# Kernel tuning notes

Measured on AMD Instinct MI355X. Metric: run time of the kernel, lower is better.

The kernel has to match this reference:

```python
import jax, jax.numpy as jnp
import numpy as np

B, L = 256, 50            # batch, n_pos (session length)
ITEM_DIM, POS_DIM = 128, 64
DIM = ITEM_DIM + POS_DIM  # 192
N_ITEMS = 50000
W = 20.0                  # temperature / init scale
LN_EPS = 1e-5


def renorm(t, max_norm=1.5):
    # torch Embedding max_norm semantics: clip row L2 norm to max_norm
    n = jnp.linalg.norm(t, axis=-1, keepdims=True)
    return t * jnp.minimum(1.0, max_norm / jnp.maximum(n, 1e-7))


def setup_inputs() -> dict:
    key = jax.random.key(0)
    ks = jax.random.split(key, 24)
    inv_w = 1.0 / W
    lb = 1.0 / np.sqrt(DIM)
    lb3 = 1.0 / np.sqrt(3 * DIM)
    u = lambda k, shape, b: jax.random.uniform(k, shape, jnp.float32, -b, b)
    emb = jax.random.normal(ks[0], (N_ITEMS, ITEM_DIM), jnp.float32).at[0].set(0.0)
    pos_emb = jax.random.normal(ks[1], (L + 1, POS_DIM), jnp.float32).at[0].set(0.0)
    return {
        'x': jax.random.randint(ks[20], (B, L), 0, N_ITEMS),
        'pos': jnp.sort(jax.random.randint(ks[21], (B, L), 1, L + 1), axis=-1),
        'emb': emb,
        'pos_emb': pos_emb,
        'vw0': jax.random.normal(ks[2], (1, DIM), jnp.float32) * inv_w,
        'vw1': jax.random.normal(ks[3], (DIM, DIM), jnp.float32) * inv_w,
        'vw2': jax.random.normal(ks[4], (DIM, DIM), jnp.float32) * inv_w,
        'vbias': jnp.zeros((DIM,), jnp.float32),
        'w1_W': u(ks[5], (DIM, DIM), lb), 'w1_b': u(ks[6], (DIM,), lb),
        'w2_W': u(ks[7], (DIM, DIM), lb), 'w2_b': u(ks[8], (DIM,), lb),
        'wA': jax.random.normal(ks[9], (1, L), jnp.float32) * inv_w,
        'wg1_W': u(ks[10], (DIM, DIM), lb), 'wg1_b': u(ks[11], (DIM,), lb),
        'wg2_W': u(ks[12], (DIM, DIM), lb), 'wg2_b': u(ks[13], (DIM,), lb),
        'gq': jax.random.normal(ks[14], (DIM, 1), jnp.float32) * inv_w,
        'wf_W': u(ks[15], (ITEM_DIM, 3 * DIM), lb3), 'wf_b': u(ks[16], (ITEM_DIM,), lb3),
        'ln_g': jnp.ones((DIM,), jnp.float32), 'ln_b': jnp.zeros((DIM,), jnp.float32),
    }


def reference(x, pos, emb, pos_emb, vw0, vw1, vw2, vbias, w1_W, w1_b, w2_W, w2_b,
              wA, wg1_W, wg1_b, wg2_W, wg2_b, gq, wf_W, wf_b, ln_g, ln_b):
    emb_r = renorm(emb)
    x_e = emb_r[x]                                   # [B,L,item_dim]
    p_e = renorm(pos_emb)[pos]                       # [B,L,pos_dim]
    x_ = jnp.concatenate([x_e, p_e], axis=-1)        # [B,L,D]
    mask = (x != 0)                                  # [B,L]

    # --- vanila (additive) attention, all n_pos targets in one fused pass ---
    K = x_ @ vw1                                     # [B,L,D]  (shared across targets)
    Q = x_ @ vw2                                     # [B,L,D]
    h = jax.nn.relu(K[:, None, :, :] + Q[:, :, None, :] + vbias)   # [B,Li,Lj,D]
    alpha = jnp.einsum('bijd,d->bij', h, vw0[0])     # scores over keys j
    alpha = jnp.where(mask[:, None, :], alpha, -jnp.inf)
    a = jax.nn.softmax(alpha, axis=-1)
    S = jnp.einsum('bij,bjd->bid', a, x_)            # [B,L,D]

    # --- MLP + LayerNorm + position mixing ---
    h2 = jax.nn.relu(S @ w1_W.T + w1_b)
    S2 = h2 @ w2_W.T + w2_b + S
    mu = jnp.mean(S2, axis=-1, keepdims=True)
    var = jnp.mean((S2 - mu) ** 2, axis=-1, keepdims=True)
    S3 = ln_g * (S2 - mu) * jax.lax.rsqrt(var + LN_EPS) + ln_b
    st = jnp.einsum('p,bpd->bd', wA[0], S3)[:, None, :]   # [B,1,D]

    # --- global attention ---
    sl = x_[:, -1:, :]                               # [B,1,D]
    g = jax.nn.sigmoid(x_ @ wg1_W.T + wg1_b + (sl @ wg2_W.T + wg2_b))
    ag = g @ gq                                      # [B,L,1]
    sg = jnp.einsum('blo,bld->bod', ag, x_)          # [B,1,D]

    # --- decoder: cosine-similarity logits against item embeddings ---
    c = jax.nn.selu(jnp.concatenate([st, sl, sg], axis=-1) @ wf_W.T + wf_b)[:, 0, :]
    c = c / jnp.linalg.norm(c, axis=-1, keepdims=True)
    le = emb_r[1:]
    le = le / jnp.linalg.norm(le, axis=-1, keepdims=True)
    z = W * (c @ le.T)                               # [B, n_items-1]
    return z
```

## Files before the change

kernel.cpp:

```cpp
#include <hip/hip_runtime.h>
#include <hip/hip_bf16.h>
#include <math.h>
#include <stdint.h>

#define BB 256
#define LL 50
#define IDIM 128
#define PDIM 64
#define DIM 192
#define NITEMS 50000
#define NOUT 49999
#define WSC 20.0f
#define EPS 1e-5f
#define WMAT (DIM * DIM)

typedef __attribute__((ext_vector_type(8))) short  short8;
typedef __attribute__((ext_vector_type(4))) float  f32x4;

__device__ __forceinline__ unsigned short f2bf(float f) {
    unsigned int u = __float_as_uint(f);
    u = (u + 0x7FFFu + ((u >> 16) & 1u)) >> 16;
    return (unsigned short)u;
}
__device__ __forceinline__ float bf2f(unsigned short u) {
    unsigned int v = ((unsigned int)u) << 16;
    return __uint_as_float(v);
}

__global__ __launch_bounds__(256) void k_norms(const float* __restrict__ emb,
                                               float* __restrict__ scale,
                                               float* __restrict__ invn,
                                               unsigned short* __restrict__ emb16) {
    int row  = blockIdx.x * 4 + (threadIdx.x >> 6);
    int lane = threadIdx.x & 63;
    const float* p = emb + (size_t)row * IDIM;
    float a = p[lane], b = p[lane + 64];
    emb16[(size_t)row * IDIM + lane]      = f2bf(a);
    emb16[(size_t)row * IDIM + lane + 64] = f2bf(b);
    float s = a * a + b * b;
#pragma unroll
    for (int off = 32; off; off >>= 1) s += __shfl_xor(s, off);
    if (lane == 0) {
        float n = sqrtf(s);
        scale[row] = fminf(1.0f, 1.5f / fmaxf(n, 1e-7f));
        invn[row]  = (n > 0.f) ? 1.f / n : 0.f;
    }
}

__global__ __launch_bounds__(64) void k_pnorms(const float* __restrict__ pe,
                                               float* __restrict__ pscale) {
    int row = threadIdx.x;
    if (row > LL) return;
    float s = 0.f;
    const float* p = pe + row * PDIM;
    for (int d = 0; d < PDIM; ++d) { float v = p[d]; s += v * v; }
    float n = sqrtf(s);
    pscale[row] = fminf(1.0f, 1.5f / fmaxf(n, 1e-7f));
}

__global__ __launch_bounds__(256) void k_cvtw(const float* __restrict__ vw1, const float* __restrict__ vw2,
                                              const float* __restrict__ w1W, const float* __restrict__ w2W,
                                              const float* __restrict__ wg1W,
                                              unsigned short* __restrict__ Wout) {
    int b = blockIdx.x;
    int wi = b / 144;
    int pos = (b % 144) * 256 + threadIdx.x;
    int n = pos / DIM, k = pos - n * DIM;
    float v;
    if      (wi == 0) v = vw1[(size_t)k * DIM + n];
    else if (wi == 1) v = vw2[(size_t)k * DIM + n];
    else if (wi == 2) v = w1W[pos];
    else if (wi == 3) v = w2W[pos];
    else              v = wg1W[pos];
    Wout[(size_t)wi * WMAT + pos] = f2bf(v);
}

__global__ __launch_bounds__(512) void k_mega(
    const int* __restrict__ x, const int* __restrict__ pos,
    const float* __restrict__ emb, const float* __restrict__ pe,
    const float* __restrict__ scale, const float* __restrict__ pscale,
    const unsigned short* __restrict__ W16,
    const float* __restrict__ vw0, const float* __restrict__ vbias,
    const float* __restrict__ w1b, const float* __restrict__ w2b,
    const float* __restrict__ wg1b, const float* __restrict__ wg2W,
    const float* __restrict__ wg2b, const float* __restrict__ gq,
    const float* __restrict__ wA, const float* __restrict__ lng,
    const float* __restrict__ lnb, const float* __restrict__ wfW,
    const float* __restrict__ wfb, unsigned short* __restrict__ Cb16g) {

    __shared__ unsigned short Bs16[64 * DIM];
    __shared__ unsigned short X16T[DIM * 72];
    __shared__ unsigned short Ab16[64 * 72];
    __shared__ float R1[LL * 196];
    __shared__ float R2[LL * 196];
    __shared__ float xlast[DIM];
    __shared__ float GLs[DIM];
    __shared__ float cvec[3 * DIM];
    __shared__ float red2[4][128];
    __shared__ float ags[64];
    __shared__ int   msk[64];
    __shared__ float was[64];
    __shared__ float red[8];
    __shared__ int   xi[LL], pii[LL];
    __shared__ float xsc[LL], psc[LL];

    const int b = blockIdx.x, t = threadIdx.x;
    const int wv = t >> 6, l = t & 63;
    const int lr = l & 15, lk = l >> 4;

    if (t < LL) {
        int v = x[b * LL + t];  xi[t] = v;  xsc[t] = scale[v];
        int pv = pos[b * LL + t]; pii[t] = pv; psc[t] = pscale[pv];
    }
    if (t >= 64 && t < 128) ags[t - 64] = 0.f;
    if (t >= 128 && t < 128 + LL) was[t - 128] = wA[t - 128];
    __syncthreads();
    if (t < 64) msk[t] = (t < LL) ? xi[t] : 0;
    for (int r = wv; r < LL; r += 8) {
        float sx = xsc[r], sp = psc[r];
        float v0 = emb[(size_t)xi[r] * IDIM + l] * sx;
        float v1 = emb[(size_t)xi[r] * IDIM + l + 64] * sx;
        float v2 = pe[pii[r] * PDIM + l] * sp;
        int base = r * 384, sw = (r & 7) << 4;
        *(unsigned short*)((char*)Bs16 + ((base + l * 2) ^ sw))         = f2bf(v0);
        *(unsigned short*)((char*)Bs16 + ((base + (l + 64) * 2) ^ sw))  = f2bf(v1);
        *(unsigned short*)((char*)Bs16 + ((base + (l + 128) * 2) ^ sw)) = f2bf(v2);
        X16T[l * 72 + r]         = f2bf(v0);
        X16T[(l + 64) * 72 + r]  = f2bf(v1);
        X16T[(l + 128) * 72 + r] = f2bf(v2);
        if (r == 49) { xlast[l] = v0; xlast[l + 64] = v1; xlast[l + 128] = v2; }
    }
    for (int e = t; e < 14 * DIM; e += 512) Bs16[LL * DIM + e] = 0;
    for (int e = t; e < DIM * 14; e += 512) { int d = e / 14, j = 50 + (e - d * 14); X16T[d * 72 + j] = 0; }
    for (int e = t; e < 14 * 72; e += 512) Ab16[50 * 72 + e] = 0;
    __syncthreads();

    if (t < DIM) {
        float g = wg2b[t];
        const float* wr = wg2W + (size_t)t * DIM;
        float s0 = 0, s1 = 0, s2 = 0, s3 = 0;
        for (int k = 0; k < DIM; k += 4) {
            float4 w4 = *(const float4*)(wr + k);
            s0 += xlast[k] * w4.x; s1 += xlast[k + 1] * w4.y;
            s2 += xlast[k + 2] * w4.z; s3 += xlast[k + 3] * w4.w;
        }
        GLs[t] = g + ((s0 + s1) + (s2 + s3));
    }
    __syncthreads();

    {
        short8 afr[4][6];
#pragma unroll
        for (int mt = 0; mt < 4; ++mt) {
            int row = mt * 16 + lr;
#pragma unroll
            for (int ks = 0; ks < 6; ++ks) {
                int byte = (row * 384 + (lk * 8 + ks * 32) * 2) ^ ((row & 7) << 4);
                afr[mt][ks] = *(const short8*)((const char*)Bs16 + byte);
            }
        }
        for (int task = wv; task < 36; task += 8) {
            int out = task / 12, nt = task % 12;
            int ncol = nt * 16 + lr;
            const unsigned short* bp = W16 + (size_t)(out == 0 ? 0 : (out == 1 ? 1 : 4)) * WMAT
                                       + (size_t)ncol * DIM + lk * 8;
            f32x4 a0 = {}, a1 = {}, a2 = {}, a3 = {};
#pragma unroll
            for (int ks = 0; ks < 6; ++ks) {
                short8 bf = *(const short8*)(bp + ks * 32);
                a0 = __builtin_amdgcn_mfma_f32_16x16x32_bf16(afr[0][ks], bf, a0, 0, 0, 0);
                a1 = __builtin_amdgcn_mfma_f32_16x16x32_bf16(afr[1][ks], bf, a1, 0, 0, 0);
                a2 = __builtin_amdgcn_mfma_f32_16x16x32_bf16(afr[2][ks], bf, a2, 0, 0, 0);
                a3 = __builtin_amdgcn_mfma_f32_16x16x32_bf16(afr[3][ks], bf, a3, 0, 0, 0);
            }
            if (out == 0) {
                float bia = vbias[ncol];
#pragma unroll
                for (int mt = 0; mt < 4; ++mt) {
                    f32x4 ac = (mt == 0) ? a0 : (mt == 1) ? a1 : (mt == 2) ? a2 : a3;
#pragma unroll
                    for (int r = 0; r < 4; ++r) {
                        int gr = mt * 16 + lk * 4 + r;
                        if (gr < LL) R1[gr * 196 + ncol] = ac[r] + bia;
                    }
                }
            } else if (out == 1) {
#pragma unroll
                for (int mt = 0; mt < 4; ++mt) {
                    f32x4 ac = (mt == 0) ? a0 : (mt == 1) ? a1 : (mt == 2) ? a2 : a3;
#pragma unroll
                    for (int r = 0; r < 4; ++r) {
                        int gr = mt * 16 + lk * 4 + r;
                        if (gr < LL) R2[gr * 196 + ncol] = ac[r];
                    }
                }
            } else {
                float bia = wg1b[ncol] + GLs[ncol];
                float gqv = gq[ncol];
#pragma unroll
                for (int mt = 0; mt < 4; ++mt) {
                    f32x4 ac = (mt == 0) ? a0 : (mt == 1) ? a1 : (mt == 2) ? a2 : a3;
                    int gr0 = mt * 16 + lk * 4;
                    float v0 = ac[0] + bia, v1 = ac[1] + bia, v2 = ac[2] + bia, v3 = ac[3] + bia;
                    float c0 = (gr0 + 0 < LL) ? gqv / (1.f + expf(-v0)) : 0.f;
                    float c1 = (gr0 + 1 < LL) ? gqv / (1.f + expf(-v1)) : 0.f;
                    float c2 = (gr0 + 2 < LL) ? gqv / (1.f + expf(-v2)) : 0.f;
                    float c3 = (gr0 + 3 < LL) ? gqv / (1.f + expf(-v3)) : 0.f;
#pragma unroll
                    for (int off = 1; off < 16; off <<= 1) {
                        c0 += __shfl_xor(c0, off); c1 += __shfl_xor(c1, off);
                        c2 += __shfl_xor(c2, off); c3 += __shfl_xor(c3, off);
                    }
                    if (lr == 0) {
                        if (gr0 + 0 < LL) atomicAdd(&ags[gr0 + 0], c0);
                        if (gr0 + 1 < LL) atomicAdd(&ags[gr0 + 1], c1);
                        if (gr0 + 2 < LL) atomicAdd(&ags[gr0 + 2], c2);
                        if (gr0 + 3 < LL) atomicAdd(&ags[gr0 + 3], c3);
                    }
                }
            }
        }
    }
    __syncthreads();

    {
        const int d0 = wv * 24;
        float kr[24], wr[24];
        {
            const float* wp = vw0 + d0;
#pragma unroll
            for (int q = 0; q < 6; ++q) {
                float4 v = *(const float4*)(wp + q * 4);
                wr[q * 4] = v.x; wr[q * 4 + 1] = v.y; wr[q * 4 + 2] = v.z; wr[q * 4 + 3] = v.w;
            }
            if (l < LL) {
                const float* kp = R1 + l * 196 + d0;
#pragma unroll
                for (int q = 0; q < 6; ++q) {
                    float4 v = *(const float4*)(kp + q * 4);
                    kr[q * 4] = v.x; kr[q * 4 + 1] = v.y; kr[q * 4 + 2] = v.z; kr[q * 4 + 3] = v.w;
                }
            } else {
#pragma unroll
                for (int q = 0; q < 24; ++q) kr[q] = 0.f;
            }
        }
        __syncthreads();
        float* parts = R1;
        const float NEG = -__builtin_inff();
        bool valid = (l < LL) && (msk[l] != 0);
        for (int i0 = 0; i0 < LL; i0 += 12) {
            int cnt = (i0 + 12 <= LL) ? 12 : (LL - i0);
            for (int i = 0; i < cnt; ++i) {
                const float* qrow = R2 + (i0 + i) * 196 + d0;
                float b0 = 0, b1 = 0, b2 = 0, b3 = 0;
#pragma unroll
                for (int q = 0; q < 6; ++q) {
                    float4 qv = *(const float4*)(qrow + q * 4);
                    b0 += fmaxf(kr[q * 4 + 0] + qv.x, 0.f) * wr[q * 4 + 0];
                    b1 += fmaxf(kr[q * 4 + 1] + qv.y, 0.f) * wr[q * 4 + 1];
                    b2 += fmaxf(kr[q * 4 + 2] + qv.z, 0.f) * wr[q * 4 + 2];
                    b3 += fmaxf(kr[q * 4 + 3] + qv.w, 0.f) * wr[q * 4 + 3];
                }
                parts[(wv * 12 + i) * 64 + l] = (b0 + b1) + (b2 + b3);
            }
            __syncthreads();
            for (int i = wv; i < cnt; i += 8) {
                float aj = 0.f;
#pragma unroll
                for (int w2 = 0; w2 < 8; ++w2) aj += parts[(w2 * 12 + i) * 64 + l];
                if (!valid) aj = NEG;
                float m = aj;
#pragma unroll
                for (int off = 32; off; off >>= 1) m = fmaxf(m, __shfl_xor(m, off));
                float e = valid ? expf(aj - m) : 0.f;
                float s = e;
#pragma unroll
                for (int off = 32; off; off >>= 1) s += __shfl_xor(s, off);
                Ab16[(i0 + i) * 72 + l] = f2bf(e / s);
            }
            __syncthreads();
        }
    }

    for (int task = wv; task < 48; task += 8) {
        int mt = task / 12, nt = task - (task / 12) * 12;
        int i0 = mt * 16, d0c = nt * 16;
        short8 aA0 = *(const short8*)(Ab16 + (i0 + lr) * 72 + lk * 8);
        short8 aA1 = *(const short8*)(Ab16 + (i0 + lr) * 72 + 32 + lk * 8);
        short8 bB0 = *(const short8*)(X16T + (d0c + lr) * 72 + lk * 8);
        short8 bB1 = *(const short8*)(X16T + (d0c + lr) * 72 + 32 + lk * 8);
        f32x4 ac = {};
        ac = __builtin_amdgcn_mfma_f32_16x16x32_bf16(aA0, bB0, ac, 0, 0, 0);
        ac = __builtin_amdgcn_mfma_f32_16x16x32_bf16(aA1, bB1, ac, 0, 0, 0);
        int d = d0c + lr;
#pragma unroll
        for (int r = 0; r < 4; ++r) {
            int i = i0 + lk * 4 + r;
            if (i < LL) {
                R2[i * 196 + d] = ac[r];
                int byte = (i * 384 + d * 2) ^ ((i & 7) << 4);
                *(unsigned short*)((char*)Bs16 + byte) = f2bf(ac[r]);
            }
        }
    }
    __syncthreads();

    {
        short8 sfr[4][6];
#pragma unroll
        for (int mt = 0; mt < 4; ++mt) {
            int row = mt * 16 + lr;
#pragma unroll
            for (int ks = 0; ks < 6; ++ks) {
                int byte = (row * 384 + (lk * 8 + ks * 32) * 2) ^ ((row & 7) << 4);
                sfr[mt][ks] = *(const short8*)((const char*)Bs16 + byte);
            }
        }
        f32x4 h0[4] = {}, h1[4] = {};
        {
            int ncol = wv * 16 + lr;
            const unsigned short* bp = W16 + (size_t)2 * WMAT + (size_t)ncol * DIM + lk * 8;
#pragma unroll
            for (int ks = 0; ks < 6; ++ks) {
                short8 bf = *(const short8*)(bp + ks * 32);
                h0[0] = __builtin_amdgcn_mfma_f32_16x16x32_bf16(sfr[0][ks], bf, h0[0], 0, 0, 0);
                h0[1] = __builtin_amdgcn_mfma_f32_16x16x32_bf16(sfr[1][ks], bf, h0[1], 0, 0, 0);
                h0[2] = __builtin_amdgcn_mfma_f32_16x16x32_bf16(sfr[2][ks], bf, h0[2], 0, 0, 0);
                h0[3] = __builtin_amdgcn_mfma_f32_16x16x32_bf16(sfr[3][ks], bf, h0[3], 0, 0, 0);
            }
        }
        if (wv < 4) {
            int ncol = (wv + 8) * 16 + lr;
            const unsigned short* bp = W16 + (size_t)2 * WMAT + (size_t)ncol * DIM + lk * 8;
#pragma unroll
            for (int ks = 0; ks < 6; ++ks) {
                short8 bf = *(const short8*)(bp + ks * 32);
                h1[0] = __builtin_amdgcn_mfma_f32_16x16x32_bf16(sfr[0][ks], bf, h1[0], 0, 0, 0);
                h1[1] = __builtin_amdgcn_mfma_f32_16x16x32_bf16(sfr[1][ks], bf, h1[1], 0, 0, 0);
                h1[2] = __builtin_amdgcn_mfma_f32_16x16x32_bf16(sfr[2][ks], bf, h1[2], 0, 0, 0);
                h1[3] = __builtin_amdgcn_mfma_f32_16x16x32_bf16(sfr[3][ks], bf, h1[3], 0, 0, 0);
            }
        }
        __syncthreads();
        {
            int gc = wv * 16 + lr;
            float bia = w1b[gc];
#pragma unroll
            for (int mt = 0; mt < 4; ++mt)
#pragma unroll
                for (int r = 0; r < 4; ++r) {
                    int gr = mt * 16 + lk * 4 + r;
                    if (gr < LL) {
                        float v = fmaxf(h0[mt][r] + bia, 0.f);
                        int byte = (gr * 384 + gc * 2) ^ ((gr & 7) << 4);
                        *(unsigned short*)((char*)Bs16 + byte) = f2bf(v);
                    }
                }
        }
        if (wv < 4) {
            int gc = (wv + 8) * 16 + lr;
            float bia = w1b[gc];
#pragma unroll
            for (int mt = 0; mt < 4; ++mt)
#pragma unroll
                for (int r = 0; r < 4; ++r) {
                    int gr = mt * 16 + lk * 4 + r;
                    if (gr < LL) {
                        float v = fmaxf(h1[mt][r] + bia, 0.f);
                        int byte = (gr * 384 + gc * 2) ^ ((gr & 7) << 4);
                        *(unsigned short*)((char*)Bs16 + byte) = f2bf(v);
                    }
                }
        }
    }
    __syncthreads();

    {
        short8 hfr[4][6];
#pragma unroll
        for (int mt = 0; mt < 4; ++mt) {
            int row = mt * 16 + lr;
#pragma unroll
            for (int ks = 0; ks < 6; ++ks) {
                int byte = (row * 384 + (lk * 8 + ks * 32) * 2) ^ ((row & 7) << 4);
                hfr[mt][ks] = *(const short8*)((const char*)Bs16 + byte);
            }
        }
        for (int nt = wv; nt < 12; nt += 8) {
            int ncol = nt * 16 + lr;
            const unsigned short* bp = W16 + (size_t)3 * WMAT + (size_t)ncol * DIM + lk * 8;
            f32x4 s0 = {}, s1 = {}, s2 = {}, s3 = {};
#pragma unroll
            for (int ks = 0; ks < 6; ++ks) {
                short8 bf = *(const short8*)(bp + ks * 32);
                s0 = __builtin_amdgcn_mfma_f32_16x16x32_bf16(hfr[0][ks], bf, s0, 0, 0, 0);
                s1 = __builtin_amdgcn_mfma_f32_16x16x32_bf16(hfr[1][ks], bf, s1, 0, 0, 0);
                s2 = __builtin_amdgcn_mfma_f32_16x16x32_bf16(hfr[2][ks], bf, s2, 0, 0, 0);
                s3 = __builtin_amdgcn_mfma_f32_16x16x32_bf16(hfr[3][ks], bf, s3, 0, 0, 0);
            }
            float bia = w2b[ncol];
#pragma unroll
            for (int mt = 0; mt < 4; ++mt) {
                f32x4 ac = (mt == 0) ? s0 : (mt == 1) ? s1 : (mt == 2) ? s2 : s3;
#pragma unroll
                for (int r = 0; r < 4; ++r) {
                    int gr = mt * 16 + lk * 4 + r;
                    if (gr < LL) R2[gr * 196 + ncol] = ac[r] + bia + R2[gr * 196 + ncol];
                }
            }
        }
    }
    __syncthreads();

    for (int r = wv; r < LL; r += 8) {
        float* p = R2 + r * 196;
        float v0 = p[l], v1 = p[l + 64], v2 = p[l + 128];
        float s = v0 + v1 + v2;
#pragma unroll
        for (int off = 32; off; off >>= 1) s += __shfl_xor(s, off);
        float mu = s * (1.f / DIM);
        float d0 = v0 - mu, d1 = v1 - mu, d2 = v2 - mu;
        float q = d0 * d0 + d1 * d1 + d2 * d2;
#pragma unroll
        for (int off = 32; off; off >>= 1) q += __shfl_xor(q, off);
        float inv = rsqrtf(q * (1.f / DIM) + EPS);
        p[l]       = lng[l] * d0 * inv + lnb[l];
        p[l + 64]  = lng[l + 64] * d1 * inv + lnb[l + 64];
        p[l + 128] = lng[l + 128] * d2 * inv + lnb[l + 128];
    }
    __syncthreads();

    if (t < DIM) {
        float st = 0.f;
        for (int p = 0; p < LL; ++p) st += was[p] * R2[p * 196 + t];
        cvec[t] = st;
        cvec[DIM + t] = xlast[t];
    } else if (t >= 320) {
        int d = t - 320;
        float sg = 0.f;
        const unsigned short* xr = X16T + d * 72;
        for (int p = 0; p < LL; ++p) sg += ags[p] * bf2f(xr[p]);
        cvec[2 * DIM + d] = sg;
    }
    __syncthreads();

    {
        int out = t & 127, part = t >> 7;
        float s = (part == 0) ? wfb[out] : 0.f;
        const float* wr = wfW + (size_t)out * (3 * DIM) + part * 144;
        const float* cv = cvec + part * 144;
        for (int e = 0; e < 144; e += 4) {
            float4 w4 = *(const float4*)(wr + e);
            s += cv[e] * w4.x + cv[e + 1] * w4.y + cv[e + 2] * w4.z + cv[e + 3] * w4.w;
        }
        red2[part][out] = s;
    }
    __syncthreads();
    float cj = 0.f;
    if (t < IDIM) {
        float s = red2[0][t] + red2[1][t] + red2[2][t] + red2[3][t];
        const float sa = 1.6732632423543772f, sc = 1.0507009873554805f;
        cj = sc * (s > 0.f ? s : sa * expm1f(s));
    }
    float sq = cj * cj;
#pragma unroll
    for (int off = 32; off; off >>= 1) sq += __shfl_xor(sq, off);
    if (l == 0) red[wv] = sq;
    __syncthreads();
    if (t < IDIM) {
        float nrm = sqrtf(red[0] + red[1]);
        Cb16g[b * IDIM + t] = f2bf(cj / nrm);
    }
}

__global__ __launch_bounds__(256) void k_z4(const unsigned short* __restrict__ Cb16,
                                            const unsigned short* __restrict__ emb16,
                                            const float* __restrict__ invn,
                                            float* __restrict__ Z) {
    __shared__ float tr[4][64][68];
    int n0 = blockIdx.x * 64;
    int t = threadIdx.x, w = t >> 6, l = t & 63;
    int lr = l & 15, lk = l >> 4;

    short8 a[4][4];
#pragma unroll
    for (int mt = 0; mt < 4; ++mt) {
        int mrow = w * 64 + mt * 16 + lr;
        const unsigned short* ap = Cb16 + (size_t)mrow * IDIM + lk * 8;
#pragma unroll
        for (int ks = 0; ks < 4; ++ks) a[mt][ks] = *(const short8*)(ap + ks * 32);
    }
    f32x4 acc[4][4] = {};
#pragma unroll
    for (int nt = 0; nt < 4; ++nt) {
        int nrow = n0 + nt * 16 + lr;
        short8 bfr[4];
        if (nrow < NOUT) {
            const unsigned short* bp = emb16 + (size_t)(nrow + 1) * IDIM + lk * 8;
#pragma unroll
            for (int ks = 0; ks < 4; ++ks) bfr[ks] = *(const short8*)(bp + ks * 32);
        } else {
            short8 z = {};
#pragma unroll
            for (int ks = 0; ks < 4; ++ks) bfr[ks] = z;
        }
#pragma unroll
        for (int mt = 0; mt < 4; ++mt)
#pragma unroll
            for (int ks = 0; ks < 4; ++ks)
                acc[mt][nt] = __builtin_amdgcn_mfma_f32_16x16x32_bf16(a[mt][ks], bfr[ks], acc[mt][nt], 0, 0, 0);
    }
#pragma unroll
    for (int nt = 0; nt < 4; ++nt) {
        int gn = n0 + nt * 16 + lr;
        float sc = (gn < NOUT) ? WSC * invn[gn + 1] : 0.f;
#pragma unroll
        for (int mt = 0; mt < 4; ++mt)
#pragma unroll
            for (int r = 0; r < 4; ++r)
                tr[w][mt * 16 + lk * 4 + r][nt * 16 + lr] = acc[mt][nt][r] * sc;
    }
    __syncthreads();
    int q = l >> 4, s = l & 15;
    bool tail = (n0 + 64) > NOUT;
#pragma unroll
    for (int it = 0; it < 16; ++it) {
        int row = it * 4 + q;
        int gm  = w * 64 + row;
        float4 v = *(const float4*)&tr[w][row][s * 4];
        if (!tail) {
            *(float4*)&Z[(size_t)gm * NOUT + n0 + s * 4] = v;
        } else {
            int c0 = n0 + s * 4;
            float vv[4] = {v.x, v.y, v.z, v.w};
#pragma unroll
            for (int j = 0; j < 4; ++j)
                if (c0 + j < NOUT) Z[(size_t)gm * NOUT + c0 + j] = vv[j];
        }
    }
}

extern "C" void kernel_launch(void* const* d_in, const int* in_sizes, int n_in,
                              void* d_out, int out_size, void* d_ws, size_t ws_size,
                              hipStream_t stream) {
    const int*   x     = (const int*)d_in[0];
    const int*   pos   = (const int*)d_in[1];
    const float* emb   = (const float*)d_in[2];
    const float* pose  = (const float*)d_in[3];
    const float* vw0   = (const float*)d_in[4];
    const float* vw1   = (const float*)d_in[5];
    const float* vw2   = (const float*)d_in[6];
    const float* vbias = (const float*)d_in[7];
    const float* w1W   = (const float*)d_in[8];
    const float* w1b   = (const float*)d_in[9];
    const float* w2W   = (const float*)d_in[10];
    const float* w2b   = (const float*)d_in[11];
    const float* wA    = (const float*)d_in[12];
    const float* wg1W  = (const float*)d_in[13];
    const float* wg1b  = (const float*)d_in[14];
    const float* wg2W  = (const float*)d_in[15];
    const float* wg2b  = (const float*)d_in[16];
    const float* gq    = (const float*)d_in[17];
    const float* wfW   = (const float*)d_in[18];
    const float* wfb   = (const float*)d_in[19];
    const float* lng   = (const float*)d_in[20];
    const float* lnb   = (const float*)d_in[21];
    float* Z = (float*)d_out;

    float* w = (float*)d_ws;
    float* scale  = w; w += NITEMS;
    float* invn   = w; w += NITEMS;
    float* pscale = w; w += 64;
    w = (float*)(((uintptr_t)w + 15) & ~(uintptr_t)15);
    unsigned short* emb16 = (unsigned short*)w; w += (size_t)NITEMS * IDIM / 2;
    unsigned short* W16   = (unsigned short*)w; w += (size_t)5 * WMAT / 2;
    unsigned short* Cb16  = (unsigned short*)w; w += (size_t)BB * IDIM / 2;

    k_norms<<<NITEMS / 4, 256, 0, stream>>>(emb, scale, invn, emb16);
    k_pnorms<<<1, 64, 0, stream>>>(pose, pscale);
    k_cvtw<<<5 * 144, 256, 0, stream>>>(vw1, vw2, w1W, w2W, wg1W, W16);
    k_mega<<<BB, 512, 0, stream>>>(x, pos, emb, pose, scale, pscale, W16,
                                   vw0, vbias, w1b, w2b, wg1b, wg2W, wg2b, gq,
                                   wA, lng, lnb, wfW, wfb, Cb16);
    k_z4<<<(NOUT + 63) / 64, 256, 0, stream>>>(Cb16, emb16, invn, Z);
}
```

Before: 109.9 us.

## Double k_mega block to 1024 threads and redistribute per-stage work across 16 waves

Launches the per-session mega kernel with 1024 threads (16 waves) instead of 512 and re-partitions each stage to use them. The two 192-column MLP GEMMs now give one 16-column tile to each of 12 waves instead of a lopsided 8+4 split. The attention-score rows are split across wave halves, and the st/sg reductions and the wf projection are split across more threads with an extra partial-sum pass. This aims to cut the serial latency of the one-block-per-batch kernel, which only launches 256 blocks, at the cost of more barriers, register pressure under launch_bounds(1024,4), and idle waves in some stages.

```diff
diff --git a/kernel.cpp b/kernel.cpp
--- a/kernel.cpp
+++ b/kernel.cpp
@@ -75,7 +75,7 @@
     Wout[(size_t)wi * WMAT + pos] = f2bf(v);
 }
 
-__global__ __launch_bounds__(512) void k_mega(
+__global__ __launch_bounds__(1024, 4) void k_mega(
     const int* __restrict__ x, const int* __restrict__ pos,
     const float* __restrict__ emb, const float* __restrict__ pe,
     const float* __restrict__ scale, const float* __restrict__ pscale,
@@ -96,11 +96,12 @@
     __shared__ float xlast[DIM];
     __shared__ float GLs[DIM];
     __shared__ float cvec[3 * DIM];
-    __shared__ float red2[4][128];
+    __shared__ float stB[DIM], sgB[DIM];
+    __shared__ float red2[8][128];
     __shared__ float ags[64];
     __shared__ int   msk[64];
     __shared__ float was[64];
-    __shared__ float red[8];
+    __shared__ float red[16];
     __shared__ int   xi[LL], pii[LL];
     __shared__ float xsc[LL], psc[LL];
 
@@ -116,7 +117,7 @@
     if (t >= 128 && t < 128 + LL) was[t - 128] = wA[t - 128];
     __syncthreads();
     if (t < 64) msk[t] = (t < LL) ? xi[t] : 0;
-    for (int r = wv; r < LL; r += 8) {
+    for (int r = wv; r < LL; r += 16) {
         float sx = xsc[r], sp = psc[r];
         float v0 = emb[(size_t)xi[r] * IDIM + l] * sx;
         float v1 = emb[(size_t)xi[r] * IDIM + l + 64] * sx;
@@ -130,9 +131,9 @@
         X16T[(l + 128) * 72 + r] = f2bf(v2);
         if (r == 49) { xlast[l] = v0; xlast[l + 64] = v1; xlast[l + 128] = v2; }
     }
-    for (int e = t; e < 14 * DIM; e += 512) Bs16[LL * DIM + e] = 0;
-    for (int e = t; e < DIM * 14; e += 512) { int d = e / 14, j = 50 + (e - d * 14); X16T[d * 72 + j] = 0; }
-    for (int e = t; e < 14 * 72; e += 512) Ab16[50 * 72 + e] = 0;
+    for (int e = t; e < 14 * DIM; e += 1024) Bs16[LL * DIM + e] = 0;
+    for (int e = t; e < DIM * 14; e += 1024) { int d = e / 14, j = 50 + (e - d * 14); X16T[d * 72 + j] = 0; }
+    for (int e = t; e < 14 * 72; e += 1024) Ab16[50 * 72 + e] = 0;
     __syncthreads();
 
     if (t < DIM) {
@@ -159,7 +160,7 @@
                 afr[mt][ks] = *(const short8*)((const char*)Bs16 + byte);
             }
         }
-        for (int task = wv; task < 36; task += 8) {
+        for (int task = wv; task < 36; task += 16) {
             int out = task / 12, nt = task % 12;
             int ncol = nt * 16 + lr;
             const unsigned short* bp = W16 + (size_t)(out == 0 ? 0 : (out == 1 ? 1 : 4)) * WMAT
@@ -224,7 +225,8 @@
     __syncthreads();
 
     {
-        const int d0 = wv * 24;
+        const int d0 = (wv & 7) * 24;
+        const int ih = wv >> 3;
         float kr[24], wr[24];
         {
             const float* wp = vw0 + d0;
@@ -251,7 +253,7 @@
         bool valid = (l < LL) && (msk[l] != 0);
         for (int i0 = 0; i0 < LL; i0 += 12) {
             int cnt = (i0 + 12 <= LL) ? 12 : (LL - i0);
-            for (int i = 0; i < cnt; ++i) {
+            for (int i = ih; i < cnt; i += 2) {
                 const float* qrow = R2 + (i0 + i) * 196 + d0;
                 float b0 = 0, b1 = 0, b2 = 0, b3 = 0;
 #pragma unroll
@@ -262,10 +264,10 @@
                     b2 += fmaxf(kr[q * 4 + 2] + qv.z, 0.f) * wr[q * 4 + 2];
                     b3 += fmaxf(kr[q * 4 + 3] + qv.w, 0.f) * wr[q * 4 + 3];
                 }
-                parts[(wv * 12 + i) * 64 + l] = (b0 + b1) + (b2 + b3);
+                parts[((wv & 7) * 12 + i) * 64 + l] = (b0 + b1) + (b2 + b3);
             }
             __syncthreads();
-            for (int i = wv; i < cnt; i += 8) {
+            for (int i = wv; i < cnt; i += 16) {
                 float aj = 0.f;
 #pragma unroll
                 for (int w2 = 0; w2 < 8; ++w2) aj += parts[(w2 * 12 + i) * 64 + l];
@@ -283,7 +285,7 @@
         }
     }
 
-    for (int task = wv; task < 48; task += 8) {
+    for (int task = wv; task < 48; task += 16) {
         int mt = task / 12, nt = task - (task / 12) * 12;
         int i0 = mt * 16, d0c = nt * 16;
         short8 aA0 = *(const short8*)(Ab16 + (i0 + lr) * 72 + lk * 8);
@@ -308,17 +310,17 @@
 
     {
         short8 sfr[4][6];
-#pragma unroll
-        for (int mt = 0; mt < 4; ++mt) {
-            int row = mt * 16 + lr;
-#pragma unroll
-            for (int ks = 0; ks < 6; ++ks) {
-                int byte = (row * 384 + (lk * 8 + ks * 32) * 2) ^ ((row & 7) << 4);
-                sfr[mt][ks] = *(const short8*)((const char*)Bs16 + byte);
-            }
-        }
-        f32x4 h0[4] = {}, h1[4] = {};
-        {
+        f32x4 h0[4] = {};
+        if (wv < 12) {
+#pragma unroll
+            for (int mt = 0; mt < 4; ++mt) {
+                int row = mt * 16 + lr;
+#pragma unroll
+                for (int ks = 0; ks < 6; ++ks) {
+                    int byte = (row * 384 + (lk * 8 + ks * 32) * 2) ^ ((row & 7) << 4);
+                    sfr[mt][ks] = *(const short8*)((const char*)Bs16 + byte);
+                }
+            }
             int ncol = wv * 16 + lr;
             const unsigned short* bp = W16 + (size_t)2 * WMAT + (size_t)ncol * DIM + lk * 8;
 #pragma unroll
@@ -330,20 +332,8 @@
                 h0[3] = __builtin_amdgcn_mfma_f32_16x16x32_bf16(sfr[3][ks], bf, h0[3], 0, 0, 0);
             }
         }
-        if (wv < 4) {
-            int ncol = (wv + 8) * 16 + lr;
-            const unsigned short* bp = W16 + (size_t)2 * WMAT + (size_t)ncol * DIM + lk * 8;
-#pragma unroll
-            for (int ks = 0; ks < 6; ++ks) {
-                short8 bf = *(const short8*)(bp + ks * 32);
-                h1[0] = __builtin_amdgcn_mfma_f32_16x16x32_bf16(sfr[0][ks], bf, h1[0], 0, 0, 0);
-                h1[1] = __builtin_amdgcn_mfma_f32_16x16x32_bf16(sfr[1][ks], bf, h1[1], 0, 0, 0);
-                h1[2] = __builtin_amdgcn_mfma_f32_16x16x32_bf16(sfr[2][ks], bf, h1[2], 0, 0, 0);
-                h1[3] = __builtin_amdgcn_mfma_f32_16x16x32_bf16(sfr[3][ks], bf, h1[3], 0, 0, 0);
-            }
-        }
         __syncthreads();
-        {
+        if (wv < 12) {
             int gc = wv * 16 + lr;
             float bia = w1b[gc];
 #pragma unroll
@@ -358,25 +348,10 @@
                     }
                 }
         }
-        if (wv < 4) {
-            int gc = (wv + 8) * 16 + lr;
-            float bia = w1b[gc];
-#pragma unroll
-            for (int mt = 0; mt < 4; ++mt)
-#pragma unroll
-                for (int r = 0; r < 4; ++r) {
-                    int gr = mt * 16 + lk * 4 + r;
-                    if (gr < LL) {
-                        float v = fmaxf(h1[mt][r] + bia, 0.f);
-                        int byte = (gr * 384 + gc * 2) ^ ((gr & 7) << 4);
-                        *(unsigned short*)((char*)Bs16 + byte) = f2bf(v);
-                    }
-                }
-        }
-    }
-    __syncthreads();
-
-    {
+    }
+    __syncthreads();
+
+    if (wv < 12) {
         short8 hfr[4][6];
 #pragma unroll
         for (int mt = 0; mt < 4; ++mt) {
@@ -387,33 +362,31 @@
                 hfr[mt][ks] = *(const short8*)((const char*)Bs16 + byte);
             }
         }
-        for (int nt = wv; nt < 12; nt += 8) {
-            int ncol = nt * 16 + lr;
-            const unsigned short* bp = W16 + (size_t)3 * WMAT + (size_t)ncol * DIM + lk * 8;
-            f32x4 s0 = {}, s1 = {}, s2 = {}, s3 = {};
-#pragma unroll
-            for (int ks = 0; ks < 6; ++ks) {
-                short8 bf = *(const short8*)(bp + ks * 32);
-                s0 = __builtin_amdgcn_mfma_f32_16x16x32_bf16(hfr[0][ks], bf, s0, 0, 0, 0);
-                s1 = __builtin_amdgcn_mfma_f32_16x16x32_bf16(hfr[1][ks], bf, s1, 0, 0, 0);
-                s2 = __builtin_amdgcn_mfma_f32_16x16x32_bf16(hfr[2][ks], bf, s2, 0, 0, 0);
-                s3 = __builtin_amdgcn_mfma_f32_16x16x32_bf16(hfr[3][ks], bf, s3, 0, 0, 0);
-            }
-            float bia = w2b[ncol];
-#pragma unroll
-            for (int mt = 0; mt < 4; ++mt) {
-                f32x4 ac = (mt == 0) ? s0 : (mt == 1) ? s1 : (mt == 2) ? s2 : s3;
-#pragma unroll
-                for (int r = 0; r < 4; ++r) {
-                    int gr = mt * 16 + lk * 4 + r;
-                    if (gr < LL) R2[gr * 196 + ncol] = ac[r] + bia + R2[gr * 196 + ncol];
-                }
-            }
-        }
-    }
-    __syncthreads();
-
-    for (int r = wv; r < LL; r += 8) {
+        int ncol = wv * 16 + lr;
+        const unsigned short* bp = W16 + (size_t)3 * WMAT + (size_t)ncol * DIM + lk * 8;
+        f32x4 s0 = {}, s1 = {}, s2 = {}, s3 = {};
+#pragma unroll
+        for (int ks = 0; ks < 6; ++ks) {
+            short8 bf = *(const short8*)(bp + ks * 32);
+            s0 = __builtin_amdgcn_mfma_f32_16x16x32_bf16(hfr[0][ks], bf, s0, 0, 0, 0);
+            s1 = __builtin_amdgcn_mfma_f32_16x16x32_bf16(hfr[1][ks], bf, s1, 0, 0, 0);
+            s2 = __builtin_amdgcn_mfma_f32_16x16x32_bf16(hfr[2][ks], bf, s2, 0, 0, 0);
+            s3 = __builtin_amdgcn_mfma_f32_16x16x32_bf16(hfr[3][ks], bf, s3, 0, 0, 0);
+        }
+        float bia = w2b[ncol];
+#pragma unroll
+        for (int mt = 0; mt < 4; ++mt) {
+            f32x4 ac = (mt == 0) ? s0 : (mt == 1) ? s1 : (mt == 2) ? s2 : s3;
+#pragma unroll
+            for (int r = 0; r < 4; ++r) {
+                int gr = mt * 16 + lk * 4 + r;
+                if (gr < LL) R2[gr * 196 + ncol] = ac[r] + bia + R2[gr * 196 + ncol];
+            }
+        }
+    }
+    __syncthreads();
+
+    for (int r = wv; r < LL; r += 16) {
         float* p = R2 + r * 196;
         float v0 = p[l], v1 = p[l + 64], v2 = p[l + 128];
         float s = v0 + v1 + v2;
@@ -433,24 +406,40 @@
 
     if (t < DIM) {
         float st = 0.f;
-        for (int p = 0; p < LL; ++p) st += was[p] * R2[p * 196 + t];
+        for (int p = 0; p < 25; ++p) st += was[p] * R2[p * 196 + t];
         cvec[t] = st;
         cvec[DIM + t] = xlast[t];
-    } else if (t >= 320) {
-        int d = t - 320;
+    } else if (t >= 256 && t < 256 + DIM) {
+        int d = t - 256;
+        float st = 0.f;
+        for (int p = 25; p < LL; ++p) st += was[p] * R2[p * 196 + d];
+        stB[d] = st;
+    } else if (t >= 512 && t < 512 + DIM) {
+        int d = t - 512;
         float sg = 0.f;
         const unsigned short* xr = X16T + d * 72;
-        for (int p = 0; p < LL; ++p) sg += ags[p] * bf2f(xr[p]);
+        for (int p = 0; p < 25; ++p) sg += ags[p] * bf2f(xr[p]);
         cvec[2 * DIM + d] = sg;
+    } else if (t >= 768 && t < 768 + DIM) {
+        int d = t - 768;
+        float sg = 0.f;
+        const unsigned short* xr = X16T + d * 72;
+        for (int p = 25; p < LL; ++p) sg += ags[p] * bf2f(xr[p]);
+        sgB[d] = sg;
+    }
+    __syncthreads();
+    if (t < DIM) {
+        cvec[t] += stB[t];
+        cvec[2 * DIM + t] += sgB[t];
     }
     __syncthreads();
 
     {
         int out = t & 127, part = t >> 7;
         float s = (part == 0) ? wfb[out] : 0.f;
-        const float* wr = wfW + (size_t)out * (3 * DIM) + part * 144;
-        const float* cv = cvec + part * 144;
-        for (int e = 0; e < 144; e += 4) {
+        const float* wr = wfW + (size_t)out * (3 * DIM) + part * 72;
+        const float* cv = cvec + part * 72;
+        for (int e = 0; e < 72; e += 4) {
             float4 w4 = *(const float4*)(wr + e);
             s += cv[e] * w4.x + cv[e + 1] * w4.y + cv[e + 2] * w4.z + cv[e + 3] * w4.w;
         }
@@ -459,14 +448,15 @@
     __syncthreads();
     float cj = 0.f;
     if (t < IDIM) {
-        float s = red2[0][t] + red2[1][t] + red2[2][t] + red2[3][t];
+        float s = red2[0][t] + red2[1][t] + red2[2][t] + red2[3][t]
+                + red2[4][t] + red2[5][t] + red2[6][t] + red2[7][t];
         const float sa = 1.6732632423543772f, sc = 1.0507009873554805f;
         cj = sc * (s > 0.f ? s : sa * expm1f(s));
     }
     float sq = cj * cj;
 #pragma unroll
     for (int off = 32; off; off >>= 1) sq += __shfl_xor(sq, off);
-    if (l == 0) red[wv] = sq;
+    if (l == 0 && wv < 2) red[wv] = sq;
     __syncthreads();
     if (t < IDIM) {
         float nrm = sqrtf(red[0] + red[1]);
@@ -580,8 +570,8 @@
     k_norms<<<NITEMS / 4, 256, 0, stream>>>(emb, scale, invn, emb16);
     k_pnorms<<<1, 64, 0, stream>>>(pose, pscale);
     k_cvtw<<<5 * 144, 256, 0, stream>>>(vw1, vw2, w1W, w2W, wg1W, W16);
-    k_mega<<<BB, 512, 0, stream>>>(x, pos, emb, pose, scale, pscale, W16,
-                                   vw0, vbias, w1b, w2b, wg1b, wg2W, wg2b, gq,
-                                   wA, lng, lnb, wfW, wfb, Cb16);
+    k_mega<<<BB, 1024, 0, stream>>>(x, pos, emb, pose, scale, pscale, W16,
+                                    vw0, vbias, w1b, w2b, wg1b, wg2W, wg2b, gq,
+                                    wA, lng, lnb, wfW, wfb, Cb16);
     k_z4<<<(NOUT + 63) / 64, 256, 0, stream>>>(Cb16, emb16, invn, Z);
 }
```

New measurement: 154.4 us. 40.5% more time.
